# Performance work log

Measured on AMD Instinct MI355X. Metric: run time of the kernel, lower is better.

The kernel has to match this reference:

```python
import jax, jax.numpy as jnp
import numpy as np

TOP_K = 2  # standard top-2 MoE gating


def setup_inputs() -> dict:
    key = jax.random.key(0)
    k1, k2, k3, k4 = jax.random.split(key, 4)
    T, D, E = 8192, 1024, 8
    x = jax.random.normal(k1, (T, D), dtype=jnp.float32)
    Wg = jax.random.normal(k2, (D, E), dtype=jnp.float32) * (1.0 / np.sqrt(D))
    We = jax.random.normal(k3, (E, D, D), dtype=jnp.float32) * (1.0 / np.sqrt(D))
    be = jax.random.normal(k4, (E, D), dtype=jnp.float32) * 0.02
    return {"x": x, "Wg": Wg, "We": We, "be": be}


def reference(x, Wg, We, be):
    # x: [T, D]; Wg: [D, E]; We: [E, D, D]; be: [E, D]
    T = x.shape[0]
    logits = x @ Wg                          # [T, E]
    probs = jax.nn.softmax(logits, axis=-1)  # [T, E]
    top_v, top_i = jax.lax.top_k(probs, TOP_K)           # [T, K]
    top_v = top_v / jnp.sum(top_v, axis=-1, keepdims=True)
    # dense combine weights [T, E] (zero for non-selected experts)
    cw = jnp.zeros_like(probs).at[jnp.arange(T)[:, None], top_i].add(top_v)
    # per-expert GEMM over all tokens (E is small), then masked combine
    h = jnp.einsum('td,edf->etf', x, We) + be[:, None, :]  # [E, T, D]
    h = jax.nn.relu(h)
    y = jnp.einsum('te,etf->tf', cw, h)                    # [T, D]
    return y
```

## Files before the change

### kernel.cpp

```cpp
#include <hip/hip_runtime.h>

#define T_TOKENS 8192
#define DMODEL   1024
#define NEXP     8

#define BM 128
#define BN 128
#define BK 64
#define NSTEP (DMODEL / BK)

typedef float f32x4  __attribute__((ext_vector_type(4)));
typedef short short8 __attribute__((ext_vector_type(8)));

__device__ __forceinline__ unsigned short f32_to_bf16(float f) {
    unsigned int u = __builtin_bit_cast(unsigned int, f);
    unsigned int r = 0x7FFFu + ((u >> 16) & 1u);
    return (unsigned short)((u + r) >> 16);
}

__global__ __launch_bounds__(256)
void we_transpose(const float* __restrict__ We, unsigned short* __restrict__ wt) {
    __shared__ unsigned short tile[64][72];
    const int e  = blockIdx.z;
    const int d0 = blockIdx.x * 64;
    const int f0 = blockIdx.y * 64;
    const float* src = We + ((size_t)e * DMODEL + d0) * DMODEL + f0;
    #pragma unroll
    for (int i = 0; i < 16; ++i) {
        int idx = i * 256 + threadIdx.x;
        int dl = idx >> 6, fl = idx & 63;
        tile[fl][dl] = f32_to_bf16(src[(size_t)dl * DMODEL + fl]);
    }
    __syncthreads();
    unsigned short* dst = wt + ((size_t)e * DMODEL + f0) * DMODEL + d0;
    #pragma unroll
    for (int i = 0; i < 16; ++i) {
        int idx = i * 256 + threadIdx.x;
        int fl = idx >> 6, dl = idx & 63;
        dst[(size_t)fl * DMODEL + dl] = tile[fl][dl];
    }
}

__global__ __launch_bounds__(256)
void gating(const float* __restrict__ x, const float* __restrict__ Wg,
            unsigned short* __restrict__ xb,
            int* __restrict__ top_e, float* __restrict__ top_w) {
    const int wave = threadIdx.x >> 6;
    const int lane = threadIdx.x & 63;
    const int t = blockIdx.x * 4 + wave;

    float lg[8];
    #pragma unroll
    for (int e = 0; e < 8; ++e) lg[e] = 0.0f;

    const float* xr = x + (size_t)t * DMODEL;
    unsigned short* xo = xb + (size_t)t * DMODEL;

    #pragma unroll
    for (int j = 0; j < 4; ++j) {
        const int d = j * 256 + lane * 4;
        float4 xv = *reinterpret_cast<const float4*>(xr + d);
        ushort4 o;
        o.x = f32_to_bf16(xv.x);
        o.y = f32_to_bf16(xv.y);
        o.z = f32_to_bf16(xv.z);
        o.w = f32_to_bf16(xv.w);
        *reinterpret_cast<ushort4*>(xo + d) = o;
        const float xs[4] = {xv.x, xv.y, xv.z, xv.w};
        #pragma unroll
        for (int c = 0; c < 4; ++c) {
            const float4 wlo = *reinterpret_cast<const float4*>(Wg + (size_t)(d + c) * 8);
            const float4 whi = *reinterpret_cast<const float4*>(Wg + (size_t)(d + c) * 8 + 4);
            lg[0] += xs[c] * wlo.x;  lg[1] += xs[c] * wlo.y;
            lg[2] += xs[c] * wlo.z;  lg[3] += xs[c] * wlo.w;
            lg[4] += xs[c] * whi.x;  lg[5] += xs[c] * whi.y;
            lg[6] += xs[c] * whi.z;  lg[7] += xs[c] * whi.w;
        }
    }
    #pragma unroll
    for (int off = 1; off < 64; off <<= 1) {
        #pragma unroll
        for (int e = 0; e < 8; ++e) lg[e] += __shfl_xor(lg[e], off);
    }

    if (lane == 0) {
        int i1 = 0; float v1 = lg[0];
        #pragma unroll
        for (int e = 1; e < 8; ++e) if (lg[e] > v1) { v1 = lg[e]; i1 = e; }
        int i2 = -1; float v2 = -1e30f;
        #pragma unroll
        for (int e = 0; e < 8; ++e) if (e != i1 && lg[e] > v2) { v2 = lg[e]; i2 = e; }
        const float w1 = 1.0f / (1.0f + __expf(v2 - v1));
        top_e[t] = i1 | (i2 << 4);
        top_w[t] = w1;
    }
}

__global__ __launch_bounds__(256)
void compact_count(const int* __restrict__ top_e, int* __restrict__ chunk_cnt) {
    const int e = blockIdx.x, c = blockIdx.y;
    const int t = c * 256 + threadIdx.x;
    const int te = top_e[t];
    const bool m = ((te & 15) == e) || (((te >> 4) & 15) == e);
    __shared__ int ws[4];
    unsigned long long b = __ballot(m);
    if ((threadIdx.x & 63) == 0) ws[threadIdx.x >> 6] = __popcll(b);
    __syncthreads();
    if (threadIdx.x == 0)
        chunk_cnt[e * 32 + c] = ws[0] + ws[1] + ws[2] + ws[3];
}

__global__ __launch_bounds__(256)
void compact_scatter(const int* __restrict__ top_e, const float* __restrict__ top_w,
                     const int* __restrict__ chunk_cnt,
                     int* __restrict__ counts, int* __restrict__ toks,
                     float* __restrict__ wgts, int* __restrict__ rows) {
    const int e    = blockIdx.x;
    const int c    = blockIdx.y;
    const int tid  = threadIdx.x;
    const int wave = tid >> 6;
    const int lane = tid & 63;

    __shared__ int sc[32];
    __shared__ int ws[4];
    if (tid < 32) sc[tid] = chunk_cnt[e * 32 + tid];

    const int t  = c * 256 + tid;
    const int te = top_e[t];
    const int e1 = te & 15;
    const int e2 = (te >> 4) & 15;
    const bool m = (e1 == e) || (e2 == e);
    const unsigned long long b = __ballot(m);
    const int pos_in_wave = __popcll(b & ((1ull << lane) - 1ull));
    if (lane == 0) ws[wave] = __popcll(b);
    __syncthreads();

    int base = 0;
    for (int i = 0; i < c; ++i) base += sc[i];
    int woff = base;
    #pragma unroll
    for (int i = 0; i < 4; ++i) if (i < wave) woff += ws[i];

    if (m) {
        const int pos = woff + pos_in_wave;
        const float w1 = top_w[t];
        toks[e * T_TOKENS + pos] = t;
        wgts[e * T_TOKENS + pos] = (e1 == e) ? w1 : 1.0f - w1;
        rows[t * 2 + ((e1 == e) ? 0 : 1)] = e * T_TOKENS + pos;
    }
    if (c == 31 && tid == 0)
        counts[e] = base + ws[0] + ws[1] + ws[2] + ws[3];
}

__global__ __launch_bounds__(256)
void expert_gemm(const unsigned short* __restrict__ xb,
                 const unsigned short* __restrict__ wt,
                 const float* __restrict__ be,
                 const int* __restrict__ counts,
                 const int* __restrict__ toks,
                 const float* __restrict__ wgts,
                 unsigned short* __restrict__ hpart) {
    const int flat = blockIdx.x + 64 * (blockIdx.y + 8 * blockIdx.z);
    const int fy   = flat & 7;
    const int rest = flat >> 3;
    const int tx   = rest & 63;
    const int e    = rest >> 6;

    const int cnt = counts[e];
    const int p0  = tx * BM;
    if (p0 >= cnt) return;
    const int f0  = fy * BN;

    __shared__ unsigned short lds_w[BN * BK];
    __shared__ unsigned short lds_x[BM * BK];
    __shared__ int   tok_s[BM];
    __shared__ float wgt_s[BM];

    const int tid  = threadIdx.x;
    const int wave = tid >> 6;
    const int lane = tid & 63;

    if (tid < BM) {
        int p = p0 + tid;
        if (p < cnt) {
            tok_s[tid] = toks[e * T_TOKENS + p];
            wgt_s[tid] = wgts[e * T_TOKENS + p];
        } else {
            tok_s[tid] = 0;
            wgt_s[tid] = 0.0f;
        }
    }
    __syncthreads();

    const char* wsrc[4];
    const char* xsrc[4];
    #pragma unroll
    for (int s = 0; s < 4; ++s) {
        const int q    = wave * 4 + s;
        const int row  = q * 8 + (lane >> 3);
        const int scol = ((lane & 7) << 4) ^ ((row & 7) << 4);
        wsrc[s] = (const char*)wt + ((size_t)(e * DMODEL + f0 + row) * DMODEL) * 2 + scol;
        xsrc[s] = (const char*)xb + ((size_t)tok_s[row] * DMODEL) * 2 + scol;
    }

    f32x4 acc[4][4] = {};

    const int wf = (wave & 1) * 64;
    const int wp = (wave >> 1) * 64;

    #pragma unroll 1
    for (int t = 0; t < NSTEP; ++t) {
        const size_t ko = (size_t)t * BK * 2;
        #pragma unroll
        for (int s = 0; s < 4; ++s) {
            __builtin_amdgcn_global_load_lds(
                (const __attribute__((address_space(1))) void*)(wsrc[s] + ko),
                (__attribute__((address_space(3))) void*)((char*)lds_w + (wave * 4 + s) * 1024),
                16, 0, 0);
            __builtin_amdgcn_global_load_lds(
                (const __attribute__((address_space(1))) void*)(xsrc[s] + ko),
                (__attribute__((address_space(3))) void*)((char*)lds_x + (wave * 4 + s) * 1024),
                16, 0, 0);
        }
        __syncthreads();

        #pragma unroll
        for (int kk = 0; kk < 2; ++kk) {
            short8 afr[4], bfr[4];
            #pragma unroll
            for (int mi = 0; mi < 4; ++mi) {
                const int row = wf + mi * 16 + (lane & 15);
                const int kb  = (kk * 64 + ((lane >> 4) << 4)) ^ ((row & 7) << 4);
                afr[mi] = *(const short8*)((const char*)lds_w + row * 128 + kb);
            }
            #pragma unroll
            for (int ni = 0; ni < 4; ++ni) {
                const int row = wp + ni * 16 + (lane & 15);
                const int kb  = (kk * 64 + ((lane >> 4) << 4)) ^ ((row & 7) << 4);
                bfr[ni] = *(const short8*)((const char*)lds_x + row * 128 + kb);
            }
            #pragma unroll
            for (int mi = 0; mi < 4; ++mi)
                #pragma unroll
                for (int ni = 0; ni < 4; ++ni)
                    asm("v_mfma_f32_16x16x32_bf16 %0, %1, %2, %0"
                        : "+v"(acc[mi][ni])
                        : "v"(afr[mi]), "v"(bfr[ni]));
        }
        __syncthreads();
    }

    #pragma unroll
    for (int ni = 0; ni < 4; ++ni) {
        const int pl = wp + ni * 16 + (lane & 15);
        const int p  = p0 + pl;
        if (p >= cnt) continue;
        const float w = wgt_s[pl];
        unsigned short* hr = hpart + (size_t)(e * T_TOKENS + p) * DMODEL + f0 + wf;
        #pragma unroll
        for (int mi = 0; mi < 4; ++mi) {
            const int fb = mi * 16 + ((lane >> 4) << 2);
            const float* ber = be + (size_t)e * DMODEL + f0 + wf + fb;
            ushort4 o;
            float v0 = acc[mi][ni][0] + ber[0]; v0 = v0 > 0.f ? v0 : 0.f;
            float v1 = acc[mi][ni][1] + ber[1]; v1 = v1 > 0.f ? v1 : 0.f;
            float v2 = acc[mi][ni][2] + ber[2]; v2 = v2 > 0.f ? v2 : 0.f;
            float v3 = acc[mi][ni][3] + ber[3]; v3 = v3 > 0.f ? v3 : 0.f;
            o.x = f32_to_bf16(v0 * w);
            o.y = f32_to_bf16(v1 * w);
            o.z = f32_to_bf16(v2 * w);
            o.w = f32_to_bf16(v3 * w);
            *reinterpret_cast<ushort4*>(hr + fb) = o;
        }
    }
}

__global__ __launch_bounds__(256)
void combine(const unsigned short* __restrict__ hpart,
             const int* __restrict__ rows,
             float* __restrict__ y) {
    const int t = blockIdx.x;
    const int r0 = rows[t * 2 + 0];
    const int r1 = rows[t * 2 + 1];
    const int f = threadIdx.x * 4;
    ushort4 a = *reinterpret_cast<const ushort4*>(hpart + (size_t)r0 * DMODEL + f);
    ushort4 b = *reinterpret_cast<const ushort4*>(hpart + (size_t)r1 * DMODEL + f);
    float4 o;
    o.x = __builtin_bit_cast(float, (unsigned)a.x << 16) + __builtin_bit_cast(float, (unsigned)b.x << 16);
    o.y = __builtin_bit_cast(float, (unsigned)a.y << 16) + __builtin_bit_cast(float, (unsigned)b.y << 16);
    o.z = __builtin_bit_cast(float, (unsigned)a.z << 16) + __builtin_bit_cast(float, (unsigned)b.z << 16);
    o.w = __builtin_bit_cast(float, (unsigned)a.w << 16) + __builtin_bit_cast(float, (unsigned)b.w << 16);
    *reinterpret_cast<float4*>(y + (size_t)t * DMODEL + f) = o;
}

extern "C" void kernel_launch(void* const* d_in, const int* in_sizes, int n_in,
                              void* d_out, int out_size, void* d_ws, size_t ws_size,
                              hipStream_t stream) {
    (void)in_sizes; (void)n_in; (void)out_size; (void)ws_size;
    const float* x  = (const float*)d_in[0];
    const float* Wg = (const float*)d_in[1];
    const float* We = (const float*)d_in[2];
    const float* be = (const float*)d_in[3];
    float* y = (float*)d_out;

    char* ws = (char*)d_ws;
    unsigned short* xb     = (unsigned short*)(ws);
    unsigned short* wt     = (unsigned short*)(ws + (16u << 20));
    size_t off = (32u << 20);
    int*   counts    = (int*)(ws + off);    off += 1024;
    int*   chunk_cnt = (int*)(ws + off);    off += 1024;
    int*   toks      = (int*)(ws + off);    off += (size_t)NEXP * T_TOKENS * 4;
    float* wgts      = (float*)(ws + off);  off += (size_t)NEXP * T_TOKENS * 4;
    int*   rows      = (int*)(ws + off);    off += (size_t)T_TOKENS * 2 * 4;
    int*   top_e     = (int*)(ws + off);    off += (size_t)T_TOKENS * 4;
    float* top_w     = (float*)(ws + off);
    unsigned short* hpart = (unsigned short*)(ws + (34u << 20));

    we_transpose<<<dim3(DMODEL / 64, DMODEL / 64, NEXP), 256, 0, stream>>>(We, wt);
    gating<<<dim3(T_TOKENS / 4), 256, 0, stream>>>(x, Wg, xb, top_e, top_w);
    compact_count<<<dim3(NEXP, 32), 256, 0, stream>>>(top_e, chunk_cnt);
    compact_scatter<<<dim3(NEXP, 32), 256, 0, stream>>>(top_e, top_w, chunk_cnt,
                                                        counts, toks, wgts, rows);
    expert_gemm<<<dim3(T_TOKENS / BM, DMODEL / BN, NEXP), 256, 0, stream>>>(
        xb, wt, be, counts, toks, wgts, hpart);
    combine<<<dim3(T_TOKENS), 256, 0, stream>>>(hpart, rows, y);
}
```

Measured before the change: 117.8 us.

## Merge prep kernels, fuse compaction count, double-buffer expert GEMM with BK 32

Merges the weight transpose and gating kernels into one launch, and folds the per-chunk counting pass into the compaction kernel, where each block recomputes its prefix by scanning top_e. The expert GEMM now uses two LDS buffers with BK halved to 32. Global-to-LDS loads for the next steps are issued while the current step computes, using explicit waitcnt and barriers. The aim is fewer launches and hiding load latency in the GEMM, at the cost of more k-steps, more barriers, and redundant top_e reads in every compaction block.

Result: slower. 122.6 us, median of 3 (+4.1%).

```diff
diff --git a/kernel.cpp b/kernel.cpp
--- a/kernel.cpp
+++ b/kernel.cpp
@@ -6,7 +6,7 @@
 
 #define BM 128
 #define BN 128
-#define BK 64
+#define BK 32
 #define NSTEP (DMODEL / BK)
 
 typedef float f32x4  __attribute__((ext_vector_type(4)));
@@ -19,111 +19,120 @@
 }
 
 __global__ __launch_bounds__(256)
-void we_transpose(const float* __restrict__ We, unsigned short* __restrict__ wt) {
+void prep(const float* __restrict__ x, const float* __restrict__ Wg,
+          const float* __restrict__ We,
+          unsigned short* __restrict__ xb, unsigned short* __restrict__ wt,
+          int* __restrict__ top_e, float* __restrict__ top_w) {
     __shared__ unsigned short tile[64][72];
-    const int e  = blockIdx.z;
-    const int d0 = blockIdx.x * 64;
-    const int f0 = blockIdx.y * 64;
-    const float* src = We + ((size_t)e * DMODEL + d0) * DMODEL + f0;
-    #pragma unroll
-    for (int i = 0; i < 16; ++i) {
-        int idx = i * 256 + threadIdx.x;
-        int dl = idx >> 6, fl = idx & 63;
-        tile[fl][dl] = f32_to_bf16(src[(size_t)dl * DMODEL + fl]);
-    }
-    __syncthreads();
-    unsigned short* dst = wt + ((size_t)e * DMODEL + f0) * DMODEL + d0;
-    #pragma unroll
-    for (int i = 0; i < 16; ++i) {
-        int idx = i * 256 + threadIdx.x;
-        int fl = idx >> 6, dl = idx & 63;
-        dst[(size_t)fl * DMODEL + dl] = tile[fl][dl];
+    const int bid = blockIdx.x;
+
+    if (bid < 2048) {
+        const int wave = threadIdx.x >> 6;
+        const int lane = threadIdx.x & 63;
+        const int t = bid * 4 + wave;
+
+        float lg[8];
+        #pragma unroll
+        for (int e = 0; e < 8; ++e) lg[e] = 0.0f;
+
+        const float* xr = x + (size_t)t * DMODEL;
+        unsigned short* xo = xb + (size_t)t * DMODEL;
+
+        #pragma unroll
+        for (int j = 0; j < 4; ++j) {
+            const int d = j * 256 + lane * 4;
+            float4 xv = *reinterpret_cast<const float4*>(xr + d);
+            ushort4 o;
+            o.x = f32_to_bf16(xv.x);
+            o.y = f32_to_bf16(xv.y);
+            o.z = f32_to_bf16(xv.z);
+            o.w = f32_to_bf16(xv.w);
+            *reinterpret_cast<ushort4*>(xo + d) = o;
+            const float xs[4] = {xv.x, xv.y, xv.z, xv.w};
+            #pragma unroll
+            for (int c = 0; c < 4; ++c) {
+                const float4 wlo = *reinterpret_cast<const float4*>(Wg + (size_t)(d + c) * 8);
+                const float4 whi = *reinterpret_cast<const float4*>(Wg + (size_t)(d + c) * 8 + 4);
+                lg[0] += xs[c] * wlo.x;  lg[1] += xs[c] * wlo.y;
+                lg[2] += xs[c] * wlo.z;  lg[3] += xs[c] * wlo.w;
+                lg[4] += xs[c] * whi.x;  lg[5] += xs[c] * whi.y;
+                lg[6] += xs[c] * whi.z;  lg[7] += xs[c] * whi.w;
+            }
+        }
+        #pragma unroll
+        for (int off = 1; off < 64; off <<= 1) {
+            #pragma unroll
+            for (int e = 0; e < 8; ++e) lg[e] += __shfl_xor(lg[e], off);
+        }
+
+        if (lane == 0) {
+            int i1 = 0; float v1 = lg[0];
+            #pragma unroll
+            for (int e = 1; e < 8; ++e) if (lg[e] > v1) { v1 = lg[e]; i1 = e; }
+            int i2 = -1; float v2 = -1e30f;
+            #pragma unroll
+            for (int e = 0; e < 8; ++e) if (e != i1 && lg[e] > v2) { v2 = lg[e]; i2 = e; }
+            const float w1 = 1.0f / (1.0f + __expf(v2 - v1));
+            top_e[t] = i1 | (i2 << 4);
+            top_w[t] = w1;
+        }
+    } else {
+        const int idx = bid - 2048;
+        const int e   = idx >> 8;
+        const int rem = idx & 255;
+        const int d0  = (rem >> 4) * 64;
+        const int f0  = (rem & 15) * 64;
+        const float* src = We + ((size_t)e * DMODEL + d0) * DMODEL + f0;
+        #pragma unroll
+        for (int i = 0; i < 16; ++i) {
+            int ix = i * 256 + threadIdx.x;
+            int dl = ix >> 6, fl = ix & 63;
+            tile[fl][dl] = f32_to_bf16(src[(size_t)dl * DMODEL + fl]);
+        }
+        __syncthreads();
+        unsigned short* dst = wt + ((size_t)e * DMODEL + f0) * DMODEL + d0;
+        #pragma unroll
+        for (int i = 0; i < 16; ++i) {
+            int ix = i * 256 + threadIdx.x;
+            int fl = ix >> 6, dl = ix & 63;
+            dst[(size_t)fl * DMODEL + dl] = tile[fl][dl];
+        }
     }
 }
 
 __global__ __launch_bounds__(256)
-void gating(const float* __restrict__ x, const float* __restrict__ Wg,
-            unsigned short* __restrict__ xb,
-            int* __restrict__ top_e, float* __restrict__ top_w) {
-    const int wave = threadIdx.x >> 6;
-    const int lane = threadIdx.x & 63;
-    const int t = blockIdx.x * 4 + wave;
-
-    float lg[8];
-    #pragma unroll
-    for (int e = 0; e < 8; ++e) lg[e] = 0.0f;
-
-    const float* xr = x + (size_t)t * DMODEL;
-    unsigned short* xo = xb + (size_t)t * DMODEL;
-
-    #pragma unroll
-    for (int j = 0; j < 4; ++j) {
-        const int d = j * 256 + lane * 4;
-        float4 xv = *reinterpret_cast<const float4*>(xr + d);
-        ushort4 o;
-        o.x = f32_to_bf16(xv.x);
-        o.y = f32_to_bf16(xv.y);
-        o.z = f32_to_bf16(xv.z);
-        o.w = f32_to_bf16(xv.w);
-        *reinterpret_cast<ushort4*>(xo + d) = o;
-        const float xs[4] = {xv.x, xv.y, xv.z, xv.w};
-        #pragma unroll
-        for (int c = 0; c < 4; ++c) {
-            const float4 wlo = *reinterpret_cast<const float4*>(Wg + (size_t)(d + c) * 8);
-            const float4 whi = *reinterpret_cast<const float4*>(Wg + (size_t)(d + c) * 8 + 4);
-            lg[0] += xs[c] * wlo.x;  lg[1] += xs[c] * wlo.y;
-            lg[2] += xs[c] * wlo.z;  lg[3] += xs[c] * wlo.w;
-            lg[4] += xs[c] * whi.x;  lg[5] += xs[c] * whi.y;
-            lg[6] += xs[c] * whi.z;  lg[7] += xs[c] * whi.w;
-        }
-    }
-    #pragma unroll
-    for (int off = 1; off < 64; off <<= 1) {
-        #pragma unroll
-        for (int e = 0; e < 8; ++e) lg[e] += __shfl_xor(lg[e], off);
-    }
-
-    if (lane == 0) {
-        int i1 = 0; float v1 = lg[0];
-        #pragma unroll
-        for (int e = 1; e < 8; ++e) if (lg[e] > v1) { v1 = lg[e]; i1 = e; }
-        int i2 = -1; float v2 = -1e30f;
-        #pragma unroll
-        for (int e = 0; e < 8; ++e) if (e != i1 && lg[e] > v2) { v2 = lg[e]; i2 = e; }
-        const float w1 = 1.0f / (1.0f + __expf(v2 - v1));
-        top_e[t] = i1 | (i2 << 4);
-        top_w[t] = w1;
-    }
-}
-
-__global__ __launch_bounds__(256)
-void compact_count(const int* __restrict__ top_e, int* __restrict__ chunk_cnt) {
-    const int e = blockIdx.x, c = blockIdx.y;
-    const int t = c * 256 + threadIdx.x;
-    const int te = top_e[t];
-    const bool m = ((te & 15) == e) || (((te >> 4) & 15) == e);
-    __shared__ int ws[4];
-    unsigned long long b = __ballot(m);
-    if ((threadIdx.x & 63) == 0) ws[threadIdx.x >> 6] = __popcll(b);
-    __syncthreads();
-    if (threadIdx.x == 0)
-        chunk_cnt[e * 32 + c] = ws[0] + ws[1] + ws[2] + ws[3];
-}
-
-__global__ __launch_bounds__(256)
-void compact_scatter(const int* __restrict__ top_e, const float* __restrict__ top_w,
-                     const int* __restrict__ chunk_cnt,
-                     int* __restrict__ counts, int* __restrict__ toks,
-                     float* __restrict__ wgts, int* __restrict__ rows) {
+void compact(const int* __restrict__ top_e, const float* __restrict__ top_w,
+             int* __restrict__ counts, int* __restrict__ toks,
+             float* __restrict__ wgts, int* __restrict__ rows) {
     const int e    = blockIdx.x;
     const int c    = blockIdx.y;
     const int tid  = threadIdx.x;
     const int wave = tid >> 6;
     const int lane = tid & 63;
 
-    __shared__ int sc[32];
+    __shared__ int sm[256];
+    __shared__ int red[4];
     __shared__ int ws[4];
-    if (tid < 32) sc[tid] = chunk_cnt[e * 32 + tid];
+
+    int mc = 0;
+    const int4* tp = reinterpret_cast<const int4*>(top_e) + tid * 8;
+    #pragma unroll
+    for (int i = 0; i < 8; ++i) {
+        int4 v = tp[i];
+        mc += (((v.x & 15) == e) || (((v.x >> 4) & 15) == e)) ? 1 : 0;
+        mc += (((v.y & 15) == e) || (((v.y >> 4) & 15) == e)) ? 1 : 0;
+        mc += (((v.z & 15) == e) || (((v.z >> 4) & 15) == e)) ? 1 : 0;
+        mc += (((v.w & 15) == e) || (((v.w >> 4) & 15) == e)) ? 1 : 0;
+    }
+    sm[tid] = mc;
+    __syncthreads();
+
+    int v = (tid < c * 8) ? sm[tid] : 0;
+    #pragma unroll
+    for (int off = 1; off < 64; off <<= 1) v += __shfl_xor(v, off);
+    if (lane == 0) red[wave] = v;
+    __syncthreads();
+    const int base = red[0] + red[1] + red[2] + red[3];
 
     const int t  = c * 256 + tid;
     const int te = top_e[t];
@@ -135,8 +144,6 @@
     if (lane == 0) ws[wave] = __popcll(b);
     __syncthreads();
 
-    int base = 0;
-    for (int i = 0; i < c; ++i) base += sc[i];
     int woff = base;
     #pragma unroll
     for (int i = 0; i < 4; ++i) if (i < wave) woff += ws[i];
@@ -171,8 +178,8 @@
     if (p0 >= cnt) return;
     const int f0  = fy * BN;
 
-    __shared__ unsigned short lds_w[BN * BK];
-    __shared__ unsigned short lds_x[BM * BK];
+    __shared__ unsigned short lds_w[2][BN * BK];
+    __shared__ unsigned short lds_x[2][BM * BK];
     __shared__ int   tok_s[BM];
     __shared__ float wgt_s[BM];
 
@@ -192,63 +199,74 @@
     }
     __syncthreads();
 
-    const char* wsrc[4];
-    const char* xsrc[4];
-    #pragma unroll
-    for (int s = 0; s < 4; ++s) {
-        const int q    = wave * 4 + s;
-        const int row  = q * 8 + (lane >> 3);
-        const int scol = ((lane & 7) << 4) ^ ((row & 7) << 4);
+    const char* wsrc[2];
+    const char* xsrc[2];
+    #pragma unroll
+    for (int s = 0; s < 2; ++s) {
+        const int q    = wave * 2 + s;
+        const int row  = q * 16 + (lane >> 2);
+        const int scol = ((lane & 3) << 4) ^ ((row & 3) << 4);
         wsrc[s] = (const char*)wt + ((size_t)(e * DMODEL + f0 + row) * DMODEL) * 2 + scol;
         xsrc[s] = (const char*)xb + ((size_t)tok_s[row] * DMODEL) * 2 + scol;
     }
 
-    f32x4 acc[4][4] = {};
-
-    const int wf = (wave & 1) * 64;
-    const int wp = (wave >> 1) * 64;
-
-    #pragma unroll 1
-    for (int t = 0; t < NSTEP; ++t) {
-        const size_t ko = (size_t)t * BK * 2;
-        #pragma unroll
-        for (int s = 0; s < 4; ++s) {
+    auto stage = [&](int buf, int step) {
+        const size_t ko = (size_t)step * (BK * 2);
+        #pragma unroll
+        for (int s = 0; s < 2; ++s) {
             __builtin_amdgcn_global_load_lds(
                 (const __attribute__((address_space(1))) void*)(wsrc[s] + ko),
-                (__attribute__((address_space(3))) void*)((char*)lds_w + (wave * 4 + s) * 1024),
+                (__attribute__((address_space(3))) void*)((char*)lds_w[buf] + (wave * 2 + s) * 1024),
                 16, 0, 0);
             __builtin_amdgcn_global_load_lds(
                 (const __attribute__((address_space(1))) void*)(xsrc[s] + ko),
-                (__attribute__((address_space(3))) void*)((char*)lds_x + (wave * 4 + s) * 1024),
+                (__attribute__((address_space(3))) void*)((char*)lds_x[buf] + (wave * 2 + s) * 1024),
                 16, 0, 0);
         }
-        __syncthreads();
-
-        #pragma unroll
-        for (int kk = 0; kk < 2; ++kk) {
-            short8 afr[4], bfr[4];
-            #pragma unroll
-            for (int mi = 0; mi < 4; ++mi) {
-                const int row = wf + mi * 16 + (lane & 15);
-                const int kb  = (kk * 64 + ((lane >> 4) << 4)) ^ ((row & 7) << 4);
-                afr[mi] = *(const short8*)((const char*)lds_w + row * 128 + kb);
-            }
-            #pragma unroll
-            for (int ni = 0; ni < 4; ++ni) {
-                const int row = wp + ni * 16 + (lane & 15);
-                const int kb  = (kk * 64 + ((lane >> 4) << 4)) ^ ((row & 7) << 4);
-                bfr[ni] = *(const short8*)((const char*)lds_x + row * 128 + kb);
-            }
-            #pragma unroll
-            for (int mi = 0; mi < 4; ++mi)
-                #pragma unroll
-                for (int ni = 0; ni < 4; ++ni)
-                    asm("v_mfma_f32_16x16x32_bf16 %0, %1, %2, %0"
-                        : "+v"(acc[mi][ni])
-                        : "v"(afr[mi]), "v"(bfr[ni]));
-        }
-        __syncthreads();
-    }
+    };
+
+    f32x4 acc[4][4] = {};
+
+    const int wf = (wave & 1) * 64;
+    const int wp = (wave >> 1) * 64;
+
+    auto compute = [&](int buf) {
+        short8 afr[4], bfr[4];
+        #pragma unroll
+        for (int mi = 0; mi < 4; ++mi) {
+            const int row = wf + mi * 16 + (lane & 15);
+            const int kb  = ((lane >> 4) << 4) ^ ((row & 3) << 4);
+            afr[mi] = *(const short8*)((const char*)lds_w[buf] + row * 64 + kb);
+        }
+        #pragma unroll
+        for (int ni = 0; ni < 4; ++ni) {
+            const int row = wp + ni * 16 + (lane & 15);
+            const int kb  = ((lane >> 4) << 4) ^ ((row & 3) << 4);
+            bfr[ni] = *(const short8*)((const char*)lds_x[buf] + row * 64 + kb);
+        }
+        #pragma unroll
+        for (int mi = 0; mi < 4; ++mi)
+            #pragma unroll
+            for (int ni = 0; ni < 4; ++ni)
+                asm("v_mfma_f32_16x16x32_bf16 %0, %1, %2, %0"
+                    : "+v"(acc[mi][ni])
+                    : "v"(afr[mi]), "v"(bfr[ni]));
+    };
+
+    stage(0, 0);
+    stage(1, 1);
+
+    #pragma unroll 1
+    for (int t = 0; t < NSTEP - 1; ++t) {
+        asm volatile("s_waitcnt vmcnt(4)" ::: "memory");
+        asm volatile("s_barrier" ::: "memory");
+        compute(t & 1);
+        asm volatile("s_barrier" ::: "memory");
+        if (t + 2 < NSTEP) stage(t & 1, t + 2);
+    }
+    asm volatile("s_waitcnt vmcnt(0)" ::: "memory");
+    asm volatile("s_barrier" ::: "memory");
+    compute((NSTEP - 1) & 1);
 
     #pragma unroll
     for (int ni = 0; ni < 4; ++ni) {
@@ -307,20 +325,16 @@
     unsigned short* xb     = (unsigned short*)(ws);
     unsigned short* wt     = (unsigned short*)(ws + (16u << 20));
     size_t off = (32u << 20);
-    int*   counts    = (int*)(ws + off);    off += 1024;
-    int*   chunk_cnt = (int*)(ws + off);    off += 1024;
-    int*   toks      = (int*)(ws + off);    off += (size_t)NEXP * T_TOKENS * 4;
-    float* wgts      = (float*)(ws + off);  off += (size_t)NEXP * T_TOKENS * 4;
-    int*   rows      = (int*)(ws + off);    off += (size_t)T_TOKENS * 2 * 4;
-    int*   top_e     = (int*)(ws + off);    off += (size_t)T_TOKENS * 4;
-    float* top_w     = (float*)(ws + off);
+    int*   counts = (int*)(ws + off);    off += 1024;
+    int*   toks   = (int*)(ws + off);    off += (size_t)NEXP * T_TOKENS * 4;
+    float* wgts   = (float*)(ws + off);  off += (size_t)NEXP * T_TOKENS * 4;
+    int*   rows   = (int*)(ws + off);    off += (size_t)T_TOKENS * 2 * 4;
+    int*   top_e  = (int*)(ws + off);    off += (size_t)T_TOKENS * 4;
+    float* top_w  = (float*)(ws + off);
     unsigned short* hpart = (unsigned short*)(ws + (34u << 20));
 
-    we_transpose<<<dim3(DMODEL / 64, DMODEL / 64, NEXP), 256, 0, stream>>>(We, wt);
-    gating<<<dim3(T_TOKENS / 4), 256, 0, stream>>>(x, Wg, xb, top_e, top_w);
-    compact_count<<<dim3(NEXP, 32), 256, 0, stream>>>(top_e, chunk_cnt);
-    compact_scatter<<<dim3(NEXP, 32), 256, 0, stream>>>(top_e, top_w, chunk_cnt,
-                                                        counts, toks, wgts, rows);
+    prep<<<dim3(4096), 256, 0, stream>>>(x, Wg, We, xb, wt, top_e, top_w);
+    compact<<<dim3(NEXP, 32), 256, 0, stream>>>(top_e, top_w, counts, toks, wgts, rows);
     expert_gemm<<<dim3(T_TOKENS / BM, DMODEL / BN, NEXP), 256, 0, stream>>>(
         xb, wt, be, counts, toks, wgts, hpart);
     combine<<<dim3(T_TOKENS), 256, 0, stream>>>(hpart, rows, y);
```
